# Kernel tuning notes

Hardware: AMD Instinct MI355X
Metric: run time of the kernel (lower is better)

The kernel has to match this reference:

```python
import jax, jax.numpy as jnp
import numpy as np

N = 8192        # number of routed items
D_IN = 1024     # sub-op output feature size (identity sub-ops)
E = 1024        # encoding_size
K = 8           # number of ops / type keys


def setup_inputs() -> dict:
    key = jax.random.key(0)
    k1, k2, k3, k4 = jax.random.split(key, 4)
    x = jax.random.normal(k1, (N, D_IN), dtype=jnp.float32)
    type_ids = jax.random.randint(k2, (N,), 0, K, dtype=jnp.int64)
    # Stacked per-type Linear params: Ws[k] maps op-k features -> encoding.
    W = jax.random.normal(k3, (K, D_IN, E), dtype=jnp.float32) / np.sqrt(D_IN)
    b = jax.random.normal(k4, (K, E), dtype=jnp.float32) * 0.01
    return {"x": x, "type_ids": type_ids, "W": W, "b": b}


def reference(x, type_ids, W, b):
    # x: [N, D], type_ids: [N] in [0, K), W: [K, D, E], b: [K, E]
    k = W.shape[0]
    onehot = jax.nn.one_hot(type_ids, k, dtype=x.dtype)          # [N, K] routing mask
    y = jnp.einsum('nd,kde->kne', x, W) + b[:, None, :]          # [K, N, E] per-type Linear
    enc = jnp.einsum('kne,nk->ne', y, onehot)                    # scatter-combine by type
    # out[:, :E] = routed encoding; out[:, E+ki] = 1.0 for item's type (one-hot tail)
    return jnp.concatenate([enc, onehot], axis=-1)               # [N, E + K]
```

## Files before the change

### kernel.cpp

```cpp
#include <hip/hip_runtime.h>

#define N_ITEMS 8192
#define D_IN    1024
#define E_OUT   1024
#define K_TYPES 8
#define OUT_W   (E_OUT + K_TYPES)

#define XBF_OFF  34816
#define WBF_OFF  (XBF_OFF + 16777216)
#define WS_NEED  ((size_t)WBF_OFF + 16777216)

typedef __attribute__((ext_vector_type(8))) short          bf16x8;
typedef __attribute__((ext_vector_type(8))) unsigned short u16x8;
typedef __attribute__((ext_vector_type(4))) float          f32x4;

__device__ __forceinline__ unsigned short f2bf(float f) {
    unsigned int u = __float_as_uint(f);
    return (unsigned short)((u + 0x7FFFu + ((u >> 16) & 1u)) >> 16);
}

__device__ __forceinline__ void gload16(const void* g, void* l) {
    __builtin_amdgcn_global_load_lds(
        (const __attribute__((address_space(1))) unsigned int*)g,
        (__attribute__((address_space(3)))       unsigned int*)l, 16, 0, 0);
}


__global__ __launch_bounds__(256) void k_sortmeta(const int* __restrict__ tid,
                                                  int* __restrict__ ws) {
    __shared__ int cnt[K_TYPES];
    const int t = threadIdx.x;
    if (t < K_TYPES) { cnt[t] = 0; ws[8 + t] = 0; }
    __syncthreads();
    int c[K_TYPES];
    #pragma unroll
    for (int k = 0; k < K_TYPES; ++k) c[k] = 0;
    for (int it = 0; it < N_ITEMS / 256; ++it) {
        const int v = tid[it * 256 + t];
        #pragma unroll
        for (int k = 0; k < K_TYPES; ++k) c[k] += (v == k) ? 1 : 0;
    }
    #pragma unroll
    for (int k = 0; k < K_TYPES; ++k) atomicAdd(&cnt[k], c[k]);
    __syncthreads();
    if (t == 0) {
        int off = 0, nt = 0;
        for (int k = 0; k < K_TYPES; ++k) {
            ws[16 + k] = off;
            const int cc = cnt[k];
            for (int r = 0; r < cc; r += 128) {
                ws[32 + 2 * nt] = k;
                ws[33 + 2 * nt] = off + r;
                ++nt;
            }
            off += cc;
        }
        ws[24] = off;
        ws[25] = nt;
    }
}

__global__ __launch_bounds__(256) void k_fused(const float* __restrict__ X,
                                               const float* __restrict__ W,
                                               const int*   __restrict__ tid,
                                               int* __restrict__ ws,
                                               float* __restrict__ out) {
    __shared__ unsigned short T[64][72];
    const int t = threadIdx.x;
    const int b = blockIdx.x;
    unsigned short* Xbf = (unsigned short*)((char*)ws + XBF_OFF);
    unsigned short* Wbf = (unsigned short*)((char*)ws + WBF_OFF);

    if (b < 1024) {
        const size_t c0 = (size_t)b * 8192 + (size_t)t * 8;
        float4 v[8];
        #pragma unroll
        for (int j = 0; j < 4; ++j) {
            v[2 * j]     = *(const float4*)(X + c0 + (size_t)j * 2048);
            v[2 * j + 1] = *(const float4*)(X + c0 + (size_t)j * 2048 + 4);
        }
        #pragma unroll
        for (int j = 0; j < 4; ++j) {
            u16x8 o;
            o[0] = f2bf(v[2 * j].x);     o[1] = f2bf(v[2 * j].y);
            o[2] = f2bf(v[2 * j].z);     o[3] = f2bf(v[2 * j].w);
            o[4] = f2bf(v[2 * j + 1].x); o[5] = f2bf(v[2 * j + 1].y);
            o[6] = f2bf(v[2 * j + 1].z); o[7] = f2bf(v[2 * j + 1].w);
            *(u16x8*)(Xbf + c0 + (size_t)j * 2048) = o;
        }
        if (b < 32) {
            const int n = b * 256 + t;
            const int v2 = tid[n];
            const int pos = ws[16 + v2] + atomicAdd(&ws[8 + v2], 1);
            ws[256 + pos] = n;
            float* o2 = out + (size_t)n * OUT_W + E_OUT;
            *(float4*)(o2)     = make_float4(v2 == 0 ? 1.f : 0.f, v2 == 1 ? 1.f : 0.f,
                                             v2 == 2 ? 1.f : 0.f, v2 == 3 ? 1.f : 0.f);
            *(float4*)(o2 + 4) = make_float4(v2 == 4 ? 1.f : 0.f, v2 == 5 ? 1.f : 0.f,
                                             v2 == 6 ? 1.f : 0.f, v2 == 7 ? 1.f : 0.f);
        }
        return;
    }

    const int tbase = (b - 1024) * 2;
    const int dl = t >> 2;
    const int eq = (t & 3) * 16;
    float4 va[2][4];
    int kk[2], dd0[2], ee0[2];
    #pragma unroll
    for (int s = 0; s < 2; ++s) {
        const int tt = tbase + s;
        kk[s]  = tt >> 8;
        const int rem = tt & 255;
        dd0[s] = (rem >> 4) << 6;
        ee0[s] = (rem & 15) << 6;
        const float* src = W + ((size_t)(kk[s] * 1024 + dd0[s] + dl)) * 1024 + ee0[s] + eq;
        #pragma unroll
        for (int q = 0; q < 4; ++q)
            va[s][q] = *(const float4*)(src + q * 4);
    }
    const int el = t >> 2;
    const int dq = (t & 3) * 16;
    #pragma unroll
    for (int s = 0; s < 2; ++s) {
        if (s) __syncthreads();
        #pragma unroll
        for (int q = 0; q < 4; ++q) {
            T[eq + q * 4 + 0][dl] = f2bf(va[s][q].x);
            T[eq + q * 4 + 1][dl] = f2bf(va[s][q].y);
            T[eq + q * 4 + 2][dl] = f2bf(va[s][q].z);
            T[eq + q * 4 + 3][dl] = f2bf(va[s][q].w);
        }
        __syncthreads();
        unsigned short* dst = Wbf + ((size_t)kk[s] << 20)
                            + (size_t)(ee0[s] + el) * 1024 + dd0[s] + dq;
        *(u16x8*)(dst)     = *(const u16x8*)&T[el][dq];
        *(u16x8*)(dst + 8) = *(const u16x8*)&T[el][dq + 8];
    }
}

__global__ __launch_bounds__(256) void k_gemm_bf16(const float* __restrict__ Bias,
                                                   const int* __restrict__ ws,
                                                   float* __restrict__ out) {
    __shared__ unsigned short As[128 * 64];
    __shared__ unsigned short Bs[128 * 64];

    const int tile = blockIdx.x;
    if (tile >= ws[25]) return;
    const int ktype     = ws[32 + 2 * tile];
    const int row_start = ws[33 + 2 * tile];
    const int rows      = min(128, ws[17 + ktype] - row_start);
    const int* __restrict__ sorted = ws + 256 + row_start;
    const int bn0 = blockIdx.y * 128;

    const unsigned short* __restrict__ Xbf =
        (const unsigned short*)((const char*)ws + XBF_OFF);
    const unsigned short* __restrict__ Wbf =
        (const unsigned short*)((const char*)ws + WBF_OFF);

    const int t    = threadIdx.x;
    const int lane = t & 63;
    const int w    = t >> 6;
    const int wr   = w >> 1, wc = w & 1;

    const int srow = lane >> 3;
    const int skq  = (lane & 7) * 8;

    const unsigned short* gA[4];
    const unsigned short* gB[4];
    unsigned short* lA[4];
    unsigned short* lB[4];
    #pragma unroll
    for (int i = 0; i < 4; ++i) {
        const int ar = w * 32 + i * 8 + srow;
        const int cr = sorted[ar < rows ? ar : rows - 1];
        gA[i] = Xbf + (size_t)cr * 1024 + skq;
        const int er = bn0 + w * 32 + i * 8 + srow;
        gB[i] = Wbf + ((size_t)ktype << 20) + (size_t)er * 1024 + skq;
        lA[i] = As + (w * 32 + i * 8) * 64;
        lB[i] = Bs + (w * 32 + i * 8) * 64;
    }

    const int frow = lane & 15;
    const int fko  = (lane >> 4) * 8;
    const unsigned short* aB = As + (wr * 64 + frow) * 64 + fko;
    const unsigned short* bBp = Bs + (wc * 64 + frow) * 64 + fko;

    f32x4 acc[4][4];
    #pragma unroll
    for (int m = 0; m < 4; ++m)
        #pragma unroll
        for (int n = 0; n < 4; ++n)
            acc[m][n] = (f32x4){0.f, 0.f, 0.f, 0.f};

    for (int k0 = 0; k0 < D_IN; k0 += 64) {
        #pragma unroll
        for (int i = 0; i < 4; ++i) {
            gload16(gA[i] + k0, lA[i]);
            gload16(gB[i] + k0, lB[i]);
        }
        __syncthreads();
        bf16x8 af[2][4], bf_[2][4];
        #pragma unroll
        for (int ks = 0; ks < 2; ++ks)
            #pragma unroll
            for (int m = 0; m < 4; ++m) {
                af[ks][m]  = *(const bf16x8*)(aB  + m * 16 * 64 + ks * 32);
                bf_[ks][m] = *(const bf16x8*)(bBp + m * 16 * 64 + ks * 32);
            }
        #pragma unroll
        for (int ks = 0; ks < 2; ++ks)
            #pragma unroll
            for (int m = 0; m < 4; ++m)
                #pragma unroll
                for (int n = 0; n < 4; ++n)
                    acc[m][n] = __builtin_amdgcn_mfma_f32_16x16x32_bf16(
                        af[ks][m], bf_[ks][n], acc[m][n], 0, 0, 0);
        __syncthreads();
    }

    const int col = lane & 15;
    const int rq  = (lane >> 4) * 4;
    float bv[4];
    #pragma unroll
    for (int n = 0; n < 4; ++n)
        bv[n] = Bias[ktype * E_OUT + bn0 + wc * 64 + n * 16 + col];
    #pragma unroll
    for (int m = 0; m < 4; ++m)
        #pragma unroll
        for (int j = 0; j < 4; ++j) {
            const int lr = wr * 64 + m * 16 + rq + j;
            if (lr < rows) {
                float* o = out + (size_t)sorted[lr] * OUT_W + bn0 + wc * 64 + col;
                o[0]  = acc[m][0][j] + bv[0];
                o[16] = acc[m][1][j] + bv[1];
                o[32] = acc[m][2][j] + bv[2];
                o[48] = acc[m][3][j] + bv[3];
            }
        }
}


__global__ void k_init(int* __restrict__ ws) {
    int t = threadIdx.x;
    if (t < K_TYPES) { ws[t] = 0; ws[8 + t] = 0; }
    if (t == 0) ws[25] = 0;
}
__global__ void k_hist(const int* __restrict__ tid, int* __restrict__ ws) {
    int n = blockIdx.x * 256 + threadIdx.x;
    if (n < N_ITEMS) atomicAdd(&ws[tid[n]], 1);
}
__global__ void k_scan(int* __restrict__ ws) {
    if (threadIdx.x != 0 || blockIdx.x != 0) return;
    int off = 0, nt = 0;
    for (int k = 0; k < K_TYPES; ++k) {
        ws[16 + k] = off;
        int c = ws[k];
        for (int r = 0; r < c; r += 128) { ws[32 + 2 * nt] = k; ws[33 + 2 * nt] = off + r; ++nt; }
        off += c;
    }
    ws[24] = off; ws[25] = nt;
}
__global__ void k_scatter(const int* __restrict__ tid, int* __restrict__ ws) {
    int n = blockIdx.x * 256 + threadIdx.x;
    if (n >= N_ITEMS) return;
    int v = tid[n];
    int pos = ws[16 + v] + atomicAdd(&ws[8 + v], 1);
    ws[256 + pos] = n;
}
__global__ void k_tail(const int* __restrict__ tid, float* __restrict__ out) {
    int i = blockIdx.x * 256 + threadIdx.x;
    if (i >= N_ITEMS * K_TYPES) return;
    int n = i >> 3, j = i & 7;
    out[(size_t)n * OUT_W + E_OUT + j] = (tid[n] == j) ? 1.0f : 0.0f;
}
__global__ __launch_bounds__(256) void k_gemm(const float* __restrict__ X,
                                              const float* __restrict__ Wt,
                                              const float* __restrict__ Bias,
                                              const int* __restrict__ ws,
                                              float* __restrict__ out) {
    const int tile = blockIdx.x;
    if (tile >= ws[25]) return;
    const int ktype = ws[32 + 2 * tile];
    const int row_start = ws[33 + 2 * tile];
    const int rows = min(128, ws[17 + ktype] - row_start);
    const int* __restrict__ sorted = ws + 256 + row_start;
    const int bn0 = blockIdx.y * 128;
    __shared__ float As2[16][132];
    __shared__ float Bs2[16][132];
    const int t = threadIdx.x, tx = t & 15, ty = t >> 4;
    const int arow0 = t >> 2, arow1 = arow0 + 64, akq = t & 3;
    const int ra = sorted[(arow0 < rows) ? arow0 : 0];
    const int rb = sorted[(arow1 < rows) ? arow1 : 0];
    const float* xa = X + (size_t)ra * D_IN + akq * 4;
    const float* xb = X + (size_t)rb * D_IN + akq * 4;
    const int bdr = t >> 5, bc = (t & 31) * 4;
    const float* wbase = Wt + ((size_t)ktype * D_IN) * E_OUT + bn0;
    const float* w0 = wbase + (size_t)bdr * E_OUT + bc;
    const float* w1 = wbase + (size_t)(bdr + 8) * E_OUT + bc;
    float acc[8][8];
    #pragma unroll
    for (int i = 0; i < 8; ++i)
        #pragma unroll
        for (int j = 0; j < 8; ++j) acc[i][j] = 0.f;
    for (int k0 = 0; k0 < D_IN; k0 += 16) {
        const float4 a0 = *(const float4*)(xa + k0);
        const float4 a1 = *(const float4*)(xb + k0);
        const float4 b0 = *(const float4*)(w0 + (size_t)k0 * E_OUT);
        const float4 b1 = *(const float4*)(w1 + (size_t)k0 * E_OUT);
        __syncthreads();
        As2[akq * 4 + 0][arow0] = a0.x; As2[akq * 4 + 1][arow0] = a0.y;
        As2[akq * 4 + 2][arow0] = a0.z; As2[akq * 4 + 3][arow0] = a0.w;
        As2[akq * 4 + 0][arow1] = a1.x; As2[akq * 4 + 1][arow1] = a1.y;
        As2[akq * 4 + 2][arow1] = a1.z; As2[akq * 4 + 3][arow1] = a1.w;
        *(float4*)&Bs2[bdr][bc] = b0; *(float4*)&Bs2[bdr + 8][bc] = b1;
        __syncthreads();
        #pragma unroll
        for (int kk = 0; kk < 16; ++kk) {
            const float4 av0 = *(const float4*)&As2[kk][ty * 4];
            const float4 av1 = *(const float4*)&As2[kk][64 + ty * 4];
            const float4 bv0 = *(const float4*)&Bs2[kk][tx * 4];
            const float4 bv1 = *(const float4*)&Bs2[kk][64 + tx * 4];
            const float a[8] = {av0.x, av0.y, av0.z, av0.w, av1.x, av1.y, av1.z, av1.w};
            const float bb[8] = {bv0.x, bv0.y, bv0.z, bv0.w, bv1.x, bv1.y, bv1.z, bv1.w};
            #pragma unroll
            for (int i = 0; i < 8; ++i)
                #pragma unroll
                for (int j = 0; j < 8; ++j) acc[i][j] = fmaf(a[i], bb[j], acc[i][j]);
        }
    }
    const float* bias = Bias + ktype * E_OUT + bn0;
    const float4 bi0 = *(const float4*)&bias[tx * 4];
    const float4 bi1 = *(const float4*)&bias[64 + tx * 4];
    const float bb[8] = {bi0.x, bi0.y, bi0.z, bi0.w, bi1.x, bi1.y, bi1.z, bi1.w};
    #pragma unroll
    for (int i = 0; i < 8; ++i) {
        const int lr = (i >> 2) * 64 + ty * 4 + (i & 3);
        if (lr < rows) {
            float* o = out + (size_t)sorted[lr] * OUT_W + bn0;
            *(float4*)&o[tx * 4] = make_float4(acc[i][0] + bb[0], acc[i][1] + bb[1],
                                               acc[i][2] + bb[2], acc[i][3] + bb[3]);
            *(float4*)&o[64 + tx * 4] = make_float4(acc[i][4] + bb[4], acc[i][5] + bb[5],
                                                    acc[i][6] + bb[6], acc[i][7] + bb[7]);
        }
    }
}

extern "C" void kernel_launch(void* const* d_in, const int* in_sizes, int n_in,
                              void* d_out, int out_size, void* d_ws, size_t ws_size,
                              hipStream_t stream) {
    const float* x   = (const float*)d_in[0];
    const int*   tid = (const int*)d_in[1];
    const float* W   = (const float*)d_in[2];
    const float* b   = (const float*)d_in[3];
    float* out = (float*)d_out;
    int*   ws  = (int*)d_ws;

    if (ws_size >= WS_NEED) {
        k_sortmeta<<<1, 256, 0, stream>>>(tid, ws);
        k_fused<<<2048, 256, 0, stream>>>(x, W, tid, ws, out);
        dim3 grid(72, 8);
        k_gemm_bf16<<<grid, 256, 0, stream>>>(b, ws, out);
    } else {
        k_init<<<1, 64, 0, stream>>>(ws);
        k_hist<<<N_ITEMS / 256, 256, 0, stream>>>(tid, ws);
        k_scan<<<1, 1, 0, stream>>>(ws);
        k_scatter<<<N_ITEMS / 256, 256, 0, stream>>>(tid, ws);
        k_tail<<<(N_ITEMS * K_TYPES) / 256, 256, 0, stream>>>(tid, out);
        dim3 grid(72, 8);
        k_gemm<<<grid, 256, 0, stream>>>(x, W, b, ws, out);
    }
}
```

Measured before the change: 214.8 us.

## Split X/W conversion kernels and halve GEMM N-tile to 64 columns

The fused conversion kernel is split into separate X-conversion and W-transpose kernels launched back to back. The bf16 GEMM tile shrinks from 128x128 to 128x64 and the grid doubles in y (72x16), so there are more workgroups and fewer accumulator registers per thread. This targets better CU occupancy and load balance across 256 CUs, at the cost of more A-tile reloads and an extra kernel launch.

```diff
diff --git a/kernel.cpp b/kernel.cpp
--- a/kernel.cpp
+++ b/kernel.cpp
@@ -60,49 +60,51 @@
     }
 }
 
-__global__ __launch_bounds__(256) void k_fused(const float* __restrict__ X,
-                                               const float* __restrict__ W,
+__global__ __launch_bounds__(256) void k_convX(const float* __restrict__ X,
                                                const int*   __restrict__ tid,
                                                int* __restrict__ ws,
                                                float* __restrict__ out) {
+    const int t = threadIdx.x;
+    const int b = blockIdx.x;
+    unsigned short* Xbf = (unsigned short*)((char*)ws + XBF_OFF);
+
+    const size_t c0 = (size_t)b * 8192 + (size_t)t * 8;
+    float4 v[8];
+    #pragma unroll
+    for (int j = 0; j < 4; ++j) {
+        v[2 * j]     = *(const float4*)(X + c0 + (size_t)j * 2048);
+        v[2 * j + 1] = *(const float4*)(X + c0 + (size_t)j * 2048 + 4);
+    }
+    #pragma unroll
+    for (int j = 0; j < 4; ++j) {
+        u16x8 o;
+        o[0] = f2bf(v[2 * j].x);     o[1] = f2bf(v[2 * j].y);
+        o[2] = f2bf(v[2 * j].z);     o[3] = f2bf(v[2 * j].w);
+        o[4] = f2bf(v[2 * j + 1].x); o[5] = f2bf(v[2 * j + 1].y);
+        o[6] = f2bf(v[2 * j + 1].z); o[7] = f2bf(v[2 * j + 1].w);
+        *(u16x8*)(Xbf + c0 + (size_t)j * 2048) = o;
+    }
+    if (b < 32) {
+        const int n = b * 256 + t;
+        const int v2 = tid[n];
+        const int pos = ws[16 + v2] + atomicAdd(&ws[8 + v2], 1);
+        ws[256 + pos] = n;
+        float* o2 = out + (size_t)n * OUT_W + E_OUT;
+        *(float4*)(o2)     = make_float4(v2 == 0 ? 1.f : 0.f, v2 == 1 ? 1.f : 0.f,
+                                         v2 == 2 ? 1.f : 0.f, v2 == 3 ? 1.f : 0.f);
+        *(float4*)(o2 + 4) = make_float4(v2 == 4 ? 1.f : 0.f, v2 == 5 ? 1.f : 0.f,
+                                         v2 == 6 ? 1.f : 0.f, v2 == 7 ? 1.f : 0.f);
+    }
+}
+
+__global__ __launch_bounds__(256) void k_convW(const float* __restrict__ W,
+                                               int* __restrict__ ws) {
     __shared__ unsigned short T[64][72];
     const int t = threadIdx.x;
     const int b = blockIdx.x;
-    unsigned short* Xbf = (unsigned short*)((char*)ws + XBF_OFF);
     unsigned short* Wbf = (unsigned short*)((char*)ws + WBF_OFF);
 
-    if (b < 1024) {
-        const size_t c0 = (size_t)b * 8192 + (size_t)t * 8;
-        float4 v[8];
-        #pragma unroll
-        for (int j = 0; j < 4; ++j) {
-            v[2 * j]     = *(const float4*)(X + c0 + (size_t)j * 2048);
-            v[2 * j + 1] = *(const float4*)(X + c0 + (size_t)j * 2048 + 4);
-        }
-        #pragma unroll
-        for (int j = 0; j < 4; ++j) {
-            u16x8 o;
-            o[0] = f2bf(v[2 * j].x);     o[1] = f2bf(v[2 * j].y);
-            o[2] = f2bf(v[2 * j].z);     o[3] = f2bf(v[2 * j].w);
-            o[4] = f2bf(v[2 * j + 1].x); o[5] = f2bf(v[2 * j + 1].y);
-            o[6] = f2bf(v[2 * j + 1].z); o[7] = f2bf(v[2 * j + 1].w);
-            *(u16x8*)(Xbf + c0 + (size_t)j * 2048) = o;
-        }
-        if (b < 32) {
-            const int n = b * 256 + t;
-            const int v2 = tid[n];
-            const int pos = ws[16 + v2] + atomicAdd(&ws[8 + v2], 1);
-            ws[256 + pos] = n;
-            float* o2 = out + (size_t)n * OUT_W + E_OUT;
-            *(float4*)(o2)     = make_float4(v2 == 0 ? 1.f : 0.f, v2 == 1 ? 1.f : 0.f,
-                                             v2 == 2 ? 1.f : 0.f, v2 == 3 ? 1.f : 0.f);
-            *(float4*)(o2 + 4) = make_float4(v2 == 4 ? 1.f : 0.f, v2 == 5 ? 1.f : 0.f,
-                                             v2 == 6 ? 1.f : 0.f, v2 == 7 ? 1.f : 0.f);
-        }
-        return;
-    }
-
-    const int tbase = (b - 1024) * 2;
+    const int tbase = b * 2;
     const int dl = t >> 2;
     const int eq = (t & 3) * 16;
     float4 va[2][4];
@@ -143,7 +145,7 @@
                                                    const int* __restrict__ ws,
                                                    float* __restrict__ out) {
     __shared__ unsigned short As[128 * 64];
-    __shared__ unsigned short Bs[128 * 64];
+    __shared__ unsigned short Bs[64 * 64];
 
     const int tile = blockIdx.x;
     if (tile >= ws[25]) return;
@@ -151,7 +153,7 @@
     const int row_start = ws[33 + 2 * tile];
     const int rows      = min(128, ws[17 + ktype] - row_start);
     const int* __restrict__ sorted = ws + 256 + row_start;
-    const int bn0 = blockIdx.y * 128;
+    const int bn0 = blockIdx.y * 64;
 
     const unsigned short* __restrict__ Xbf =
         (const unsigned short*)((const char*)ws + XBF_OFF);
@@ -167,53 +169,57 @@
     const int skq  = (lane & 7) * 8;
 
     const unsigned short* gA[4];
-    const unsigned short* gB[4];
     unsigned short* lA[4];
-    unsigned short* lB[4];
     #pragma unroll
     for (int i = 0; i < 4; ++i) {
         const int ar = w * 32 + i * 8 + srow;
         const int cr = sorted[ar < rows ? ar : rows - 1];
         gA[i] = Xbf + (size_t)cr * 1024 + skq;
-        const int er = bn0 + w * 32 + i * 8 + srow;
+        lA[i] = As + (w * 32 + i * 8) * 64;
+    }
+    const unsigned short* gB[2];
+    unsigned short* lB[2];
+    #pragma unroll
+    for (int i = 0; i < 2; ++i) {
+        const int er = bn0 + w * 16 + i * 8 + srow;
         gB[i] = Wbf + ((size_t)ktype << 20) + (size_t)er * 1024 + skq;
-        lA[i] = As + (w * 32 + i * 8) * 64;
-        lB[i] = Bs + (w * 32 + i * 8) * 64;
+        lB[i] = Bs + (w * 16 + i * 8) * 64;
     }
 
     const int frow = lane & 15;
     const int fko  = (lane >> 4) * 8;
-    const unsigned short* aB = As + (wr * 64 + frow) * 64 + fko;
-    const unsigned short* bBp = Bs + (wc * 64 + frow) * 64 + fko;
-
-    f32x4 acc[4][4];
+    const unsigned short* aB  = As + (wr * 64 + frow) * 64 + fko;
+    const unsigned short* bBp = Bs + (wc * 32 + frow) * 64 + fko;
+
+    f32x4 acc[4][2];
     #pragma unroll
     for (int m = 0; m < 4; ++m)
         #pragma unroll
-        for (int n = 0; n < 4; ++n)
+        for (int n = 0; n < 2; ++n)
             acc[m][n] = (f32x4){0.f, 0.f, 0.f, 0.f};
 
     for (int k0 = 0; k0 < D_IN; k0 += 64) {
         #pragma unroll
-        for (int i = 0; i < 4; ++i) {
-            gload16(gA[i] + k0, lA[i]);
-            gload16(gB[i] + k0, lB[i]);
-        }
-        __syncthreads();
-        bf16x8 af[2][4], bf_[2][4];
-        #pragma unroll
-        for (int ks = 0; ks < 2; ++ks)
+        for (int i = 0; i < 4; ++i) gload16(gA[i] + k0, lA[i]);
+        #pragma unroll
+        for (int i = 0; i < 2; ++i) gload16(gB[i] + k0, lB[i]);
+        __syncthreads();
+        bf16x8 af[2][4], bf_[2][2];
+        #pragma unroll
+        for (int ks = 0; ks < 2; ++ks) {
             #pragma unroll
-            for (int m = 0; m < 4; ++m) {
+            for (int m = 0; m < 4; ++m)
                 af[ks][m]  = *(const bf16x8*)(aB  + m * 16 * 64 + ks * 32);
-                bf_[ks][m] = *(const bf16x8*)(bBp + m * 16 * 64 + ks * 32);
-            }
+            #pragma unroll
+            for (int n = 0; n < 2; ++n)
+                bf_[ks][n] = *(const bf16x8*)(bBp + n * 16 * 64 + ks * 32);
+        }
         #pragma unroll
         for (int ks = 0; ks < 2; ++ks)
             #pragma unroll
             for (int m = 0; m < 4; ++m)
                 #pragma unroll
-                for (int n = 0; n < 4; ++n)
+                for (int n = 0; n < 2; ++n)
                     acc[m][n] = __builtin_amdgcn_mfma_f32_16x16x32_bf16(
                         af[ks][m], bf_[ks][n], acc[m][n], 0, 0, 0);
         __syncthreads();
@@ -221,21 +227,19 @@
 
     const int col = lane & 15;
     const int rq  = (lane >> 4) * 4;
-    float bv[4];
-    #pragma unroll
-    for (int n = 0; n < 4; ++n)
-        bv[n] = Bias[ktype * E_OUT + bn0 + wc * 64 + n * 16 + col];
+    float bv[2];
+    #pragma unroll
+    for (int n = 0; n < 2; ++n)
+        bv[n] = Bias[ktype * E_OUT + bn0 + wc * 32 + n * 16 + col];
     #pragma unroll
     for (int m = 0; m < 4; ++m)
         #pragma unroll
         for (int j = 0; j < 4; ++j) {
             const int lr = wr * 64 + m * 16 + rq + j;
             if (lr < rows) {
-                float* o = out + (size_t)sorted[lr] * OUT_W + bn0 + wc * 64 + col;
+                float* o = out + (size_t)sorted[lr] * OUT_W + bn0 + wc * 32 + col;
                 o[0]  = acc[m][0][j] + bv[0];
                 o[16] = acc[m][1][j] + bv[1];
-                o[32] = acc[m][2][j] + bv[2];
-                o[48] = acc[m][3][j] + bv[3];
             }
         }
 }
@@ -358,8 +362,9 @@
 
     if (ws_size >= WS_NEED) {
         k_sortmeta<<<1, 256, 0, stream>>>(tid, ws);
-        k_fused<<<2048, 256, 0, stream>>>(x, W, tid, ws, out);
-        dim3 grid(72, 8);
+        k_convX<<<1024, 256, 0, stream>>>(x, tid, ws, out);
+        k_convW<<<1024, 256, 0, stream>>>(W, ws);
+        dim3 grid(72, 16);
         k_gemm_bf16<<<grid, 256, 0, stream>>>(b, ws, out);
     } else {
         k_init<<<1, 64, 0, stream>>>(ws);
```

Measured after the change: 215.6 us. Within noise of the previous version (+0.4%).
